# Kernel tuning notes

Measured on AMD Instinct MI355X. Metric: run time of the kernel, lower is better.

Reference implementation:

```python
import jax, jax.numpy as jnp
import numpy as np

BN = 1.0 / np.sqrt(1.0 + 1e-5)  # eval-mode BatchNorm at init (mean=0,var=1,gamma=1,beta=0)
EPS = 1e-5
WIN = 5
NH, HD = 8, 6

def _conv2d(x, w, ph, pw, groups=1):
    return jax.lax.conv_general_dilated(x, w, (1, 1), ((ph, ph), (pw, pw)),
        dimension_numbers=('NCHW', 'OIHW', 'NCHW'), feature_group_count=groups)

def _conv1d(x, w, p, groups=1):
    return jax.lax.conv_general_dilated(x, w, (1,), ((p, p),),
        dimension_numbers=('NCH', 'OIH', 'NCH'), feature_group_count=groups)

def _avgpool_t(x, k):
    s = jax.lax.reduce_window(x, 0.0, jax.lax.add, (1, 1, 1, k), (1, 1, 1, k), 'VALID')
    return s / k

def _ln(h, g, b):
    m = h.mean(-1, keepdims=True)
    v = h.var(-1, keepdims=True)  # biased, matches torch LayerNorm
    return (h - m) / jnp.sqrt(v + EPS) * g + b

def setup_inputs() -> dict:
    ks = jax.random.split(jax.random.key(0), 20)
    def n(i, shape, s=0.05):
        return jax.random.normal(ks[i], shape, dtype=jnp.float32) * s
    z = lambda *s: jnp.zeros(s, jnp.float32)
    o = lambda *s: jnp.ones(s, jnp.float32)
    return {
        'x': jax.random.normal(ks[0], (16, 1, 22, 16000), dtype=jnp.float32),
        'riem_w1': n(1, (253, 256)), 'riem_b1': z(256),
        'riem_w2': n(2, (256, 48)), 'riem_b2': z(48),
        'conv1_w': n(3, (16, 1, 1, 64)),
        'dw1_w': n(4, (32, 1, 22, 1)),
        'dw2_w': n(5, (32, 1, 1, 16)),
        'pw_w': n(6, (48, 32, 1, 1)),
        'tc1_w': n(7, (24, 2, 3)), 'tc1_b': z(24),
        'tc2_w': n(8, (48, 24, 1)), 'tc2_b': z(48),
        'fusion_proj': n(9, (48, 48), 0.15),
        'pos_enc': n(10, (1, 500, 48), 0.02),
        'ln1_g': o(4, 48), 'ln1_b': z(4, 48),
        'qkv_w': n(11, (4, 48, 144)), 'qkv_b': z(4, 144),
        'attn_proj_w': n(12, (4, 48, 48)), 'attn_proj_b': z(4, 48),
        'ln2_g': o(4, 48), 'ln2_b': z(4, 48),
        'ffn_w1': n(13, (4, 48, 192)), 'ffn_b1': z(4, 192),
        'ffn_w2': n(14, (4, 192, 48)), 'ffn_b2': z(4, 48),
        'cls_ln_g': o(48), 'cls_ln_b': z(48),
        'cls_w': n(15, (48, 4), 0.1), 'cls_b': z(4),
    }

def _forward(x, riem_w1, riem_b1, riem_w2, riem_b2, conv1_w, dw1_w, dw2_w, pw_w,
             tc1_w, tc1_b, tc2_w, tc2_b, fusion_proj, pos_enc,
             ln1_g, ln1_b, qkv_w, qkv_b, attn_proj_w, attn_proj_b,
             ln2_g, ln2_b, ffn_w1, ffn_b1, ffn_w2, ffn_b2,
             cls_ln_g, cls_ln_b, cls_w, cls_b):
    B = x.shape[0]
    # ---- Riemannian geometry branch ----
    xr = x[:, 0]                                   # (B, 22, T)
    C, T = xr.shape[1], xr.shape[2]
    xc = xr - xr.mean(-1, keepdims=True)
    cov = jnp.einsum('bct,bdt->bcd', xc, xc) / (T - 1)
    I = jnp.eye(C, dtype=x.dtype)
    cov = cov + I * 1e-5
    tr = jnp.trace(cov, axis1=1, axis2=2)
    cov = cov + I * (tr.mean() * 1e-3)
    L = jnp.linalg.cholesky(cov)
    dL = jnp.diagonal(L, axis1=-2, axis2=-1)
    log_cov = L * jnp.log(jnp.clip(dL, 1e-10))[:, None, :]   # L @ diag(log(diag L))
    iu = jnp.triu_indices(C)
    flat = log_cov[:, iu[0], iu[1]]                # (B, 253)
    r_feat = (jax.nn.elu(flat @ riem_w1 + riem_b1) @ riem_w2 + riem_b2)[:, None, :]
    # ---- Lightweight CNN branch (BatchNorms in eval = constant scale) ----
    h = _conv2d(x, conv1_w, 0, 32) * BN
    h = jax.nn.elu(_conv2d(h, dw1_w, 0, 0, groups=16) * BN)
    h = _avgpool_t(h, 8)
    h = _conv2d(h, dw2_w, 0, 8, groups=32) * BN
    h = jax.nn.elu(_conv2d(h, pw_w, 0, 0) * BN)
    h = _avgpool_t(h, 8)                            # (B, 48, 1, L)
    feat = jnp.transpose(h[:, :, 0, :], (0, 2, 1))  # (B, L, 48)
    t = _conv1d(jnp.transpose(feat, (0, 2, 1)), tc1_w, 1, groups=24) + tc1_b[None, :, None]
    t = jax.nn.gelu(t * BN, approximate=False)
    t = _conv1d(t, tc2_w, 0) + tc2_b[None, :, None]
    feat = feat + jnp.transpose(t, (0, 2, 1))
    # ---- Fusion + positional encoding ----
    fused = jnp.concatenate([r_feat, feat], axis=1) @ fusion_proj
    N = fused.shape[1]
    fused = fused + pos_enc[:, :N]
    # ---- Sparse (banded) transformer blocks ----
    idx = jnp.arange(N)
    band = jnp.abs(idx[:, None] - idx[None, :]) <= WIN   # allowed positions
    scale = HD ** -0.5
    for i in range(4):
        res = fused
        hh = _ln(fused, ln1_g[i], ln1_b[i])
        qkv = (hh @ qkv_w[i] + qkv_b[i]).reshape(B, N, 3, NH, HD)
        q = jnp.transpose(qkv[:, :, 0], (0, 2, 1, 3))
        k = jnp.transpose(qkv[:, :, 1], (0, 2, 1, 3))
        v = jnp.transpose(qkv[:, :, 2], (0, 2, 1, 3))
        att = jnp.einsum('bhqd,bhkd->bhqk', q, k) * scale
        att = jax.nn.softmax(jnp.where(band, att, -jnp.inf), axis=-1)
        o = jnp.einsum('bhqk,bhkd->bhqd', att, v)
        o = jnp.transpose(o, (0, 2, 1, 3)).reshape(B, N, NH * HD)
        fused = res + (o @ attn_proj_w[i] + attn_proj_b[i])
        res = fused
        hh = _ln(fused, ln2_g[i], ln2_b[i])
        hh = jax.nn.gelu(hh @ ffn_w1[i] + ffn_b1[i], approximate=False) @ ffn_w2[i] + ffn_b2[i]
        fused = res + hh
    g = fused.mean(axis=1)
    g = _ln(g, cls_ln_g, cls_ln_b)
    return g @ cls_w + cls_b

def reference(x, riem_w1, riem_b1, riem_w2, riem_b2, conv1_w, dw1_w, dw2_w, pw_w,
              tc1_w, tc1_b, tc2_w, tc2_b, fusion_proj, pos_enc,
              ln1_g, ln1_b, qkv_w, qkv_b, attn_proj_w, attn_proj_b,
              ln2_g, ln2_b, ffn_w1, ffn_b1, ffn_w2, ffn_b2,
              cls_ln_g, cls_ln_b, cls_w, cls_b):
    return _forward(x, riem_w1, riem_b1, riem_w2, riem_b2, conv1_w, dw1_w, dw2_w, pw_w,
                    tc1_w, tc1_b, tc2_w, tc2_b, fusion_proj, pos_enc,
                    ln1_g, ln1_b, qkv_w, qkv_b, attn_proj_w, attn_proj_b,
                    ln2_g, ln2_b, ffn_w1, ffn_b1, ffn_w2, ffn_b2,
                    cls_ln_g, cls_ln_b, cls_w, cls_b)
```

## Files before the change

### kernel.cpp

```cpp
#include <hip/hip_runtime.h>
#include <hip/hip_bf16.h>
#include <math.h>

#define BN_C 0.9999950000375f
#define NB 16
#define NC 22
#define NT 16000
#define NPAIR 253
#define NSEQ 251
#define ND 48
#define TR 8
#define TE 18

__device__ __forceinline__ unsigned short f2bf(float f) {
    union { float f; unsigned int u; } v; v.f = f;
    unsigned int r = v.u + 0x7fff + ((v.u >> 16) & 1);
    return (unsigned short)(r >> 16);
}
__device__ __forceinline__ float bf2f(unsigned short s) {
    union { unsigned int u; float f; } v; v.u = ((unsigned int)s) << 16;
    return v.f;
}
__device__ __forceinline__ float elu_fast(float z) {
    return (z > 0.f) ? z : (__expf(z) - 1.f);
}

#define TCHUNK 500
#define XROW 504
__global__ __launch_bounds__(256) void k_ycov(const float* __restrict__ x,
                                              const float* __restrict__ dw1,
                                              __hip_bfloat16* __restrict__ y,
                                              float* __restrict__ covS,
                                              float* __restrict__ sums) {
    __shared__ unsigned short xs[NC * XROW];
    if (blockIdx.x < 512) {
        int chunk = blockIdx.x & 31, b = blockIdx.x >> 5;
        int t0 = chunk * TCHUNK;
        const float* xp = x + (size_t)b * NC * NT + t0;
        for (int i = threadIdx.x; i < NC * 126; i += 256) {
            int c = i / 126, q = i % 126;
            unsigned long long pk = 0ull;
            if (q < 125) {
                float4 v = *(const float4*)&xp[(size_t)c * NT + 4 * q];
                pk = (unsigned long long)f2bf(v.x) | ((unsigned long long)f2bf(v.y) << 16)
                   | ((unsigned long long)f2bf(v.z) << 32) | ((unsigned long long)f2bf(v.w) << 48);
            }
            *(unsigned long long*)&xs[c * XROW + 4 * q] = pk;
        }
        __syncthreads();
        int p = threadIdx.x;
        if (p < NPAIR) {
            int c = 0, r = p;
            while (r >= NC - c) { r -= NC - c; c++; }
            int d = c + r;
            const unsigned short* xc = &xs[c * XROW];
            const unsigned short* xd = &xs[d * XROW];
            float a0 = 0, a1 = 0, a2 = 0, a3 = 0;
            float s0 = 0, s1 = 0, s2 = 0, s3 = 0;
            for (int t = 0; t < XROW; t += 8) {
                uint4 pc = *(const uint4*)&xc[t];
                uint4 pd = *(const uint4*)&xd[t];
                float c0 = bf2f((unsigned short)pc.x), c1 = bf2f((unsigned short)(pc.x >> 16));
                float c2 = bf2f((unsigned short)pc.y), c3 = bf2f((unsigned short)(pc.y >> 16));
                float c4 = bf2f((unsigned short)pc.z), c5 = bf2f((unsigned short)(pc.z >> 16));
                float c6 = bf2f((unsigned short)pc.w), c7 = bf2f((unsigned short)(pc.w >> 16));
                float d0 = bf2f((unsigned short)pd.x), d1 = bf2f((unsigned short)(pd.x >> 16));
                float d2 = bf2f((unsigned short)pd.y), d3 = bf2f((unsigned short)(pd.y >> 16));
                float d4 = bf2f((unsigned short)pd.z), d5 = bf2f((unsigned short)(pd.z >> 16));
                float d6 = bf2f((unsigned short)pd.w), d7 = bf2f((unsigned short)(pd.w >> 16));
                a0 += c0 * d0 + c4 * d4; a1 += c1 * d1 + c5 * d5;
                a2 += c2 * d2 + c6 * d6; a3 += c3 * d3 + c7 * d7;
                s0 += c0 + c4; s1 += c1 + c5; s2 += c2 + c6; s3 += c3 + c7;
            }
            atomicAdd(&covS[b * NPAIR + p], (a0 + a1) + (a2 + a3));
            if (c == d) atomicAdd(&sums[b * NC + c], (s0 + s1) + (s2 + s3));
        }
    } else {
        int gid = (blockIdx.x - 512) * 256 + threadIdx.x;
        int b = gid / 8000, tp = gid % 8000;
        int t = tp * 2;
        const float* xb = x + (size_t)b * NC * NT + t;
        float a0[32], a1[32];
        #pragma unroll
        for (int j = 0; j < 32; j++) { a0[j] = 0.f; a1[j] = 0.f; }
        for (int h = 0; h < NC; h++) {
            float2 xv = *(const float2*)&xb[(size_t)h * NT];
            #pragma unroll
            for (int j = 0; j < 32; j++) {
                float w = dw1[j * NC + h];
                a0[j] += w * xv.x; a1[j] += w * xv.y;
            }
        }
        unsigned int* yo = (unsigned int*)(y + (size_t)b * 32 * NT + t);
        #pragma unroll
        for (int j = 0; j < 32; j++) {
            unsigned int pk = (unsigned int)f2bf(a0[j]) | ((unsigned int)f2bf(a1[j]) << 16);
            yo[j * (NT / 2)] = pk;
        }
    }
}

__global__ __launch_bounds__(256) void k_convchol(
    const __hip_bfloat16* __restrict__ y, const float* __restrict__ c1w,
    float* __restrict__ p,
    const float* __restrict__ covS, const float* __restrict__ sums,
    const float* __restrict__ w1, const float* __restrict__ b1,
    const float* __restrict__ w2, const float* __restrict__ b2,
    float* __restrict__ rfeat) {
    __shared__ float4 yt4[528];
    __shared__ float covL[484];
    __shared__ float trS[NB];
    __shared__ float dvs[NC];
    __shared__ float hid[256];
    __shared__ float part[4][ND];
    if (blockIdx.x < 4096) {
        int tile = blockIdx.x & 7, j = (blockIdx.x >> 3) & 31, b = blockIdx.x >> 8;
        int u0 = tile * 256;
        const __hip_bfloat16* yp = y + ((size_t)(b * 32 + j)) * NT;
        int tbase = u0 * 8 - 32;
        for (int w = threadIdx.x; w < 528; w += 256) {
            int tq = tbase + 4 * w;
            float4 v;
            if (tq >= 0 && tq + 3 < NT) {
                uint2 pk = *(const uint2*)(yp + tq);
                v.x = bf2f((unsigned short)pk.x); v.y = bf2f((unsigned short)(pk.x >> 16));
                v.z = bf2f((unsigned short)pk.y); v.w = bf2f((unsigned short)(pk.y >> 16));
            } else {
                v.x = (tq >= 0 && tq < NT) ? __bfloat162float(yp[tq]) : 0.f;
                v.y = (tq + 1 >= 0 && tq + 1 < NT) ? __bfloat162float(yp[tq + 1]) : 0.f;
                v.z = (tq + 2 >= 0 && tq + 2 < NT) ? __bfloat162float(yp[tq + 2]) : 0.f;
                v.w = (tq + 3 >= 0 && tq + 3 < NT) ? __bfloat162float(yp[tq + 3]) : 0.f;
            }
            yt4[w ^ ((w >> 3) & 1)] = v;
        }
        __syncthreads();
        const float* cf = c1w + (j >> 1) * 64;
        int u = u0 + threadIdx.x;
        if (u < 2000) {
            float acc[8];
            #pragma unroll
            for (int s = 0; s < 8; s++) acc[s] = 0.f;
            #pragma unroll
            for (int kb = 0; kb < 64; kb += 16) {
                int B0 = 2 * threadIdx.x + (kb >> 2);
                float Yb[24];
                #pragma unroll
                for (int q = 0; q < 6; q++) {
                    int w = B0 + q;
                    float4 v = yt4[w ^ ((w >> 3) & 1)];
                    Yb[4 * q] = v.x; Yb[4 * q + 1] = v.y;
                    Yb[4 * q + 2] = v.z; Yb[4 * q + 3] = v.w;
                }
                #pragma unroll
                for (int k = 0; k < 16; k++) {
                    float c = cf[kb + k];
                    #pragma unroll
                    for (int s = 0; s < 8; s++) acc[s] += c * Yb[k + s];
                }
            }
            const float bn2 = BN_C * BN_C;
            float pv = 0.f;
            #pragma unroll
            for (int s = 0; s < 8; s++) pv += elu_fast(bn2 * acc[s]);
            p[((size_t)(b * 32 + j)) * 2000 + u] = pv * 0.125f;
        }
    } else {
        int b = blockIdx.x - 4096, t = threadIdx.x;
        if (t < NB) trS[t] = 0.f;
        __syncthreads();
        if (t < NPAIR) {
            int c = 0, r = t;
            while (r >= NC - c) { r -= NC - c; c++; }
            int d = c + r;
            float v = (covS[b * NPAIR + t] - sums[b * NC + c] * sums[b * NC + d] / (float)NT)
                      / (float)(NT - 1);
            if (c == d) v += 1e-5f;
            covL[c * NC + d] = v;
            covL[d * NC + c] = v;
        }
        for (int i = t; i < NB * NC; i += 256) {
            int bb = i / NC, c = i % NC;
            int pos = c * NC - c * (c - 1) / 2;
            float sc = sums[bb * NC + c];
            float v = (covS[bb * NPAIR + pos] - sc * sc / (float)NT) / (float)(NT - 1) + 1e-5f;
            atomicAdd(&trS[bb], v);
        }
        __syncthreads();
        float trs = 0.f;
        for (int i = 0; i < NB; i++) trs += trS[i];
        float trm = trs * (0.001f / (float)NB);
        if (t < 64) {
            int lane = t;
            float a[NC];
            #pragma unroll
            for (int j = 0; j < NC; j++) {
                float v = (lane < NC) ? covL[lane * NC + j] : 0.f;
                a[j] = v + ((j == lane) ? trm : 0.f);
            }
            float diagv = 1.f;
            #pragma unroll
            for (int k = 0; k < NC; k++) {
                float akk = __shfl(a[k], k);
                float dk = sqrtf(akk);
                if (lane == k) { a[k] = dk; diagv = dk; }
                else if (lane > k) a[k] /= dk;
                float myak = a[k];
                #pragma unroll
                for (int j = k + 1; j < NC; j++) {
                    float ljk = __shfl(myak, j);
                    if (lane >= j) a[j] -= myak * ljk;
                }
            }
            if (lane < NC) dvs[lane] = diagv * logf(fmaxf(diagv, 1e-10f));
        }
        __syncthreads();
        {
            float acc = b1[t];
            #pragma unroll
            for (int d = 0; d < NC; d++) {
                int pos = d * NC - d * (d - 1) / 2;
                acc += dvs[d] * w1[pos * 256 + t];
            }
            hid[t] = elu_fast(acc);
        }
        __syncthreads();
        if (t < 192) {
            int col = t % ND, kc = t / ND;
            float a = 0.f;
            #pragma unroll
            for (int i = 0; i < 64; i++) a += hid[kc * 64 + i] * w2[(kc * 64 + i) * ND + col];
            part[kc][col] = a;
        }
        __syncthreads();
        if (t < ND)
            rfeat[b * ND + t] = b2[t] + part[0][t] + part[1][t] + part[2][t] + part[3][t];
    }
}

__global__ __launch_bounds__(256) void k_stage2(const float* __restrict__ p,
                                                const float* __restrict__ dw2,
                                                const float* __restrict__ pw,
                                                float* __restrict__ feat) {
    int u2b = blockIdx.x * 4, b = blockIdx.y, t = threadIdx.x;
    __shared__ float pt[32][48];
    __shared__ float dval[32][32];
    __shared__ float w2s[512];
    __shared__ float pws[1536];
    for (int i = t; i < 512; i += 256) w2s[i] = dw2[i];
    for (int i = t; i < 1536; i += 256) pws[i] = pw[i];
    int base = 8 * u2b - 8;
    for (int i = t; i < 32 * 47; i += 256) {
        int j = i / 47, tt = i % 47;
        int gt = base + tt;
        pt[j][tt] = (gt >= 0 && gt < 2000) ? p[((size_t)(b * 32 + j)) * 2000 + gt] : 0.f;
    }
    __syncthreads();
    for (int i = t; i < 1024; i += 256) {
        int j = i >> 5, su = i & 31;
        int u = su >> 3, s = su & 7;
        float a = 0.f;
        #pragma unroll
        for (int k = 0; k < 16; k++) a += w2s[j * 16 + k] * pt[j][8 * u + s + k];
        dval[j][su] = a * BN_C;
    }
    __syncthreads();
    if (t < 192) {
        int col = t % ND, u = t / ND;
        int u2 = u2b + u;
        if (u2 < 250) {
            float wreg[32];
            #pragma unroll
            for (int j = 0; j < 32; j++) wreg[j] = pws[col * 32 + j];
            float acc = 0.f;
            #pragma unroll
            for (int s = 0; s < 8; s++) {
                float e = 0.f;
                #pragma unroll
                for (int j = 0; j < 32; j++) e += wreg[j] * dval[j][u * 8 + s];
                acc += elu_fast(e * BN_C);
            }
            feat[((size_t)b * 250 + u2) * ND + col] = acc * 0.125f;
        }
    }
}

__global__ __launch_bounds__(256) void k_fuse(
    const float* __restrict__ feat, const float* __restrict__ rfeat,
    const float* __restrict__ tc1w, const float* __restrict__ tc1b,
    const float* __restrict__ tc2w, const float* __restrict__ tc2b,
    const float* __restrict__ fp, const float* __restrict__ pe,
    float* __restrict__ fused) {
    int b = blockIdx.y;
    int sub = threadIdx.x >> 6, lt = threadIdx.x & 63;
    int n = blockIdx.x * 4 + sub;
    bool valid = (n < NSEQ);
    __shared__ float row[4][ND];
    __shared__ float g1[4][24];
    if (valid) {
        if (n == 0) {
            if (lt < ND) row[sub][lt] = rfeat[b * ND + lt];
        } else {
            int u = n - 1;
            if (lt < 24) {
                int m = lt;
                float a = tc1b[m];
                #pragma unroll
                for (int k = 0; k < 3; k++) {
                    int uu = u + k - 1;
                    if (uu >= 0 && uu < 250) {
                        float f0 = feat[((size_t)b * 250 + uu) * ND + 2 * m];
                        float f1 = feat[((size_t)b * 250 + uu) * ND + 2 * m + 1];
                        a += tc1w[m * 6 + k] * f0 + tc1w[m * 6 + 3 + k] * f1;
                    }
                }
                float z = a * BN_C;
                g1[sub][m] = 0.5f * z * (1.f + erff(z * 0.70710678f));
            }
        }
    }
    __syncthreads();
    if (valid && n > 0 && lt < ND) {
        int u = n - 1;
        float a = tc2b[lt];
        #pragma unroll
        for (int m = 0; m < 24; m++) a += tc2w[lt * 24 + m] * g1[sub][m];
        row[sub][lt] = feat[((size_t)b * 250 + u) * ND + lt] + a;
    }
    __syncthreads();
    if (valid && lt < ND) {
        float o = pe[n * ND + lt];
        for (int c = 0; c < ND; c++) o += row[sub][c] * fp[c * ND + lt];
        fused[((size_t)b * NSEQ + n) * ND + lt] = o;
    }
}

__global__ __launch_bounds__(512) void k_layer(
    float* __restrict__ fused,
    const float* __restrict__ g1v, const float* __restrict__ b1v,
    const float* __restrict__ qw, const float* __restrict__ qb,
    const float* __restrict__ apw, const float* __restrict__ apb,
    const float* __restrict__ g2v, const float* __restrict__ b2v,
    const float* __restrict__ w1, const float* __restrict__ fb1,
    const float* __restrict__ w2, const float* __restrict__ fb2) {
    int tile = blockIdx.x, b = blockIdx.y;
    int n0 = tile * TR;
    int t = threadIdx.x;
    __shared__ float row[TE][ND];
    __shared__ float hh[TE][ND];
    __shared__ float qkvS[TE * 144];
    __shared__ float ob[TR][ND];
    __shared__ float nrow[TR][ND];
    __shared__ float mrs[TE][2];
    __shared__ float part[4][TR][ND];
    float* hid = qkvS;

    for (int i = t; i < TE * ND; i += 512) {
        int e = i / ND, c = i % ND;
        int n = n0 - 5 + e;
        row[e][c] = (n >= 0 && n < NSEQ) ? fused[((size_t)b * NSEQ + n) * ND + c] : 0.f;
    }
    __syncthreads();
    if (t < TE * 16) {
        int r = t >> 4, i = t & 15;
        float v0 = row[r][i], v1 = row[r][i + 16], v2 = row[r][i + 32];
        float s = v0 + v1 + v2;
        s += __shfl_down(s, 8, 16); s += __shfl_down(s, 4, 16);
        s += __shfl_down(s, 2, 16); s += __shfl_down(s, 1, 16);
        float m = __shfl(s, 0, 16) * (1.f / ND);
        float d0 = v0 - m, d1 = v1 - m, d2 = v2 - m;
        float q = d0 * d0 + d1 * d1 + d2 * d2;
        q += __shfl_down(q, 8, 16); q += __shfl_down(q, 4, 16);
        q += __shfl_down(q, 2, 16); q += __shfl_down(q, 1, 16);
        if (i == 0) { mrs[r][0] = m; mrs[r][1] = rsqrtf(q * (1.f / ND) + 1e-5f); }
    }
    __syncthreads();
    for (int i = t; i < TE * ND; i += 512) {
        int e = i / ND, c = i % ND;
        hh[e][c] = (row[e][c] - mrs[e][0]) * mrs[e][1] * g1v[c] + b1v[c];
    }
    __syncthreads();
    if (t < 288) {
        int col = t % 144, eg = t / 144;
        float w[ND];
        #pragma unroll
        for (int c = 0; c < ND; c++) w[c] = qw[c * 144 + col];
        float bias = qb[col];
        for (int e = eg * 9; e < eg * 9 + 9; e++) {
            float a = bias;
            #pragma unroll
            for (int c = 0; c < ND; c++) a += hh[e][c] * w[c];
            qkvS[e * 144 + col] = a;
        }
    }
    __syncthreads();
    if (t < TR * 8) {
        int r = t >> 3, h = t & 7;
        int n = n0 + r;
        if (n < NSEQ) {
            int k0 = n - 5; if (k0 < 0) k0 = 0;
            int k1 = n + 5; if (k1 > NSEQ - 1) k1 = NSEQ - 1;
            int nk = k1 - k0 + 1;
            float q[6];
            #pragma unroll
            for (int d = 0; d < 6; d++) q[d] = qkvS[(r + 5) * 144 + h * 6 + d];
            float sc[11];
            float mx = -1e30f;
            for (int ki = 0; ki < nk; ki++) {
                int e = k0 + ki - n0 + 5;
                float s = 0;
                #pragma unroll
                for (int d = 0; d < 6; d++) s += q[d] * qkvS[e * 144 + 48 + h * 6 + d];
                s *= 0.4082482904638631f;
                sc[ki] = s; mx = fmaxf(mx, s);
            }
            float sum = 0;
            for (int ki = 0; ki < nk; ki++) { float e = __expf(sc[ki] - mx); sc[ki] = e; sum += e; }
            float inv = 1.f / sum;
            float o[6] = {0, 0, 0, 0, 0, 0};
            for (int ki = 0; ki < nk; ki++) {
                int e = k0 + ki - n0 + 5;
                float pv = sc[ki] * inv;
                #pragma unroll
                for (int d = 0; d < 6; d++) o[d] += pv * qkvS[e * 144 + 96 + h * 6 + d];
            }
            #pragma unroll
            for (int d = 0; d < 6; d++) ob[r][h * 6 + d] = o[d];
        } else {
            #pragma unroll
            for (int d = 0; d < 6; d++) ob[r][h * 6 + d] = 0.f;
        }
    }
    __syncthreads();
    if (t < TR * ND) {
        int r = t / ND, col = t % ND;
        float a = apb[col];
        #pragma unroll
        for (int c = 0; c < ND; c++) a += ob[r][c] * apw[c * ND + col];
        nrow[r][col] = row[r + 5][col] + a;
    }
    __syncthreads();
    if (t < TR * 16) {
        int r = t >> 4, i = t & 15;
        float v0 = nrow[r][i], v1 = nrow[r][i + 16], v2 = nrow[r][i + 32];
        float s = v0 + v1 + v2;
        s += __shfl_down(s, 8, 16); s += __shfl_down(s, 4, 16);
        s += __shfl_down(s, 2, 16); s += __shfl_down(s, 1, 16);
        float m = __shfl(s, 0, 16) * (1.f / ND);
        float d0 = v0 - m, d1 = v1 - m, d2 = v2 - m;
        float q = d0 * d0 + d1 * d1 + d2 * d2;
        q += __shfl_down(q, 8, 16); q += __shfl_down(q, 4, 16);
        q += __shfl_down(q, 2, 16); q += __shfl_down(q, 1, 16);
        if (i == 0) { mrs[r][0] = m; mrs[r][1] = rsqrtf(q * (1.f / ND) + 1e-5f); }
    }
    __syncthreads();
    if (t < TR * ND) {
        int r = t / ND, c = t % ND;
        hh[r][c] = (nrow[r][c] - mrs[r][0]) * mrs[r][1] * g2v[c] + b2v[c];
    }
    __syncthreads();
    if (t < 384) {
        int col = t % 192, rg = t / 192;
        float w[ND];
        #pragma unroll
        for (int c = 0; c < ND; c++) w[c] = w1[c * 192 + col];
        float bias = fb1[col];
        for (int r = rg * 4; r < rg * 4 + 4; r++) {
            float a = bias;
            #pragma unroll
            for (int c = 0; c < ND; c++) a += hh[r][c] * w[c];
            hid[r * 192 + col] = 0.5f * a * (1.f + erff(a * 0.70710678f));
        }
    }
    __syncthreads();
    if (t < 384) {
        int col = t % ND, kc = (t / ND) & 3, rh = t / 192;
        float w[ND];
        #pragma unroll
        for (int i2 = 0; i2 < ND; i2++) w[i2] = w2[(kc * ND + i2) * ND + col];
        for (int r = rh * 4; r < rh * 4 + 4; r++) {
            float a = 0;
            #pragma unroll
            for (int i2 = 0; i2 < ND; i2++) a += hid[r * 192 + kc * ND + i2] * w[i2];
            part[kc][r][col] = a;
        }
    }
    __syncthreads();
    for (int i = t; i < TR * ND; i += 512) {
        int r = i / ND, c = i % ND;
        int n = n0 + r;
        if (n < NSEQ) {
            fused[((size_t)b * NSEQ + n) * ND + c] =
                nrow[r][c] + fb2[c] + part[0][r][c] + part[1][r][c] + part[2][r][c] + part[3][r][c];
        }
    }
}

__global__ void k_head(const float* __restrict__ fused, const float* __restrict__ lg,
                       const float* __restrict__ lb, const float* __restrict__ cw,
                       const float* __restrict__ cb, float* __restrict__ out) {
    int b = blockIdx.x, t = threadIdx.x;
    __shared__ float part[4][ND];
    __shared__ float gg[ND], mv[2];
    if (t < 192) {
        int col = t % ND, qt = t / ND;
        int nA = qt * 63;
        int nB = (nA + 63 < NSEQ) ? nA + 63 : NSEQ;
        float s = 0.f;
        for (int n = nA; n < nB; n++) s += fused[((size_t)b * NSEQ + n) * ND + col];
        part[qt][col] = s;
    }
    __syncthreads();
    if (t < ND) gg[t] = (part[0][t] + part[1][t] + part[2][t] + part[3][t]) * (1.f / NSEQ);
    __syncthreads();
    if (t == 0) {
        float m = 0;
        for (int c = 0; c < ND; c++) m += gg[c];
        m /= (float)ND;
        float v = 0;
        for (int c = 0; c < ND; c++) { float dd = gg[c] - m; v += dd * dd; }
        v /= (float)ND;
        mv[0] = m; mv[1] = rsqrtf(v + 1e-5f);
    }
    __syncthreads();
    if (t < ND) gg[t] = (gg[t] - mv[0]) * mv[1] * lg[t] + lb[t];
    __syncthreads();
    if (t < 4) {
        float a = cb[t];
        for (int c = 0; c < ND; c++) a += gg[c] * cw[c * 4 + t];
        out[b * 4 + t] = a;
    }
}

extern "C" void kernel_launch(void* const* d_in, const int* in_sizes, int n_in,
                              void* d_out, int out_size, void* d_ws, size_t ws_size,
                              hipStream_t stream) {
    const float* x       = (const float*)d_in[0];
    const float* riem_w1 = (const float*)d_in[1];
    const float* riem_b1 = (const float*)d_in[2];
    const float* riem_w2 = (const float*)d_in[3];
    const float* riem_b2 = (const float*)d_in[4];
    const float* conv1_w = (const float*)d_in[5];
    const float* dw1_w   = (const float*)d_in[6];
    const float* dw2_w   = (const float*)d_in[7];
    const float* pw_w    = (const float*)d_in[8];
    const float* tc1_w   = (const float*)d_in[9];
    const float* tc1_b   = (const float*)d_in[10];
    const float* tc2_w   = (const float*)d_in[11];
    const float* tc2_b   = (const float*)d_in[12];
    const float* fusion  = (const float*)d_in[13];
    const float* pos_enc = (const float*)d_in[14];
    const float* ln1_g   = (const float*)d_in[15];
    const float* ln1_b   = (const float*)d_in[16];
    const float* qkv_w   = (const float*)d_in[17];
    const float* qkv_b   = (const float*)d_in[18];
    const float* apw     = (const float*)d_in[19];
    const float* apb     = (const float*)d_in[20];
    const float* ln2_g   = (const float*)d_in[21];
    const float* ln2_b   = (const float*)d_in[22];
    const float* ffn_w1  = (const float*)d_in[23];
    const float* ffn_b1  = (const float*)d_in[24];
    const float* ffn_w2  = (const float*)d_in[25];
    const float* ffn_b2  = (const float*)d_in[26];
    const float* cls_g   = (const float*)d_in[27];
    const float* cls_b_  = (const float*)d_in[28];
    const float* cls_w   = (const float*)d_in[29];
    const float* cls_bb  = (const float*)d_in[30];
    float* out = (float*)d_out;

    float* ws = (float*)d_ws;
    float* covS  = ws;
    float* sums  = ws + 4048;
    float* rfeat = ws + 4400;
    float* feat  = ws + 5168;
    float* fused = ws + 197168;
    float* pbuf  = ws + 389936;
    __hip_bfloat16* ybuf = (__hip_bfloat16*)(ws + 1413936);

    hipMemsetAsync(covS, 0, 4400 * sizeof(float), stream);

    k_ycov<<<1012, 256, 0, stream>>>(x, dw1_w, ybuf, covS, sums);
    k_convchol<<<4112, 256, 0, stream>>>(ybuf, conv1_w, pbuf, covS, sums,
                                         riem_w1, riem_b1, riem_w2, riem_b2, rfeat);
    k_stage2<<<dim3(63, NB), 256, 0, stream>>>(pbuf, dw2_w, pw_w, feat);
    k_fuse<<<dim3(63, NB), 256, 0, stream>>>(feat, rfeat, tc1_w, tc1_b, tc2_w, tc2_b,
                                             fusion, pos_enc, fused);

    for (int i = 0; i < 4; i++) {
        k_layer<<<dim3(32, NB), 512, 0, stream>>>(
            fused, ln1_g + i * 48, ln1_b + i * 48, qkv_w + i * 6912, qkv_b + i * 144,
            apw + i * 2304, apb + i * 48, ln2_g + i * 48, ln2_b + i * 48,
            ffn_w1 + i * 9216, ffn_b1 + i * 192, ffn_w2 + i * 9216, ffn_b2 + i * 48);
    }

    k_head<<<NB, 256, 0, stream>>>(fused, cls_g, cls_b_, cls_w, cls_bb, out);
}
```

Before: 273.5 us.

## Use padded scalar LDS layout for conv tile and schedule Cholesky blocks first

Replaces the XOR-swizzled float4 shared-memory tile with a scalar float array padded by one slot every eight elements, loaded with 32-bit bf16-pair reads and read back one element at a time. The aim is to avoid LDS bank conflicts in the convolution inner loop. It also moves the 16 covariance/Cholesky blocks to the start of the grid so the long serial blocks launch first rather than last. In exchange the shared-memory reads go from 6 wide loads to 23 scalar loads per chunk, which may add LDS instruction overhead.

```diff
diff --git a/kernel.cpp b/kernel.cpp
--- a/kernel.cpp
+++ b/kernel.cpp
@@ -107,49 +107,48 @@
     const float* __restrict__ w1, const float* __restrict__ b1,
     const float* __restrict__ w2, const float* __restrict__ b2,
     float* __restrict__ rfeat) {
-    __shared__ float4 yt4[528];
+    __shared__ float yt[2376];
     __shared__ float covL[484];
     __shared__ float trS[NB];
     __shared__ float dvs[NC];
     __shared__ float hid[256];
     __shared__ float part[4][ND];
-    if (blockIdx.x < 4096) {
-        int tile = blockIdx.x & 7, j = (blockIdx.x >> 3) & 31, b = blockIdx.x >> 8;
+    if (blockIdx.x >= NB) {
+        int bx = blockIdx.x - NB;
+        int tile = bx & 7, j = (bx >> 3) & 31, b = bx >> 8;
         int u0 = tile * 256;
         const __hip_bfloat16* yp = y + ((size_t)(b * 32 + j)) * NT;
         int tbase = u0 * 8 - 32;
-        for (int w = threadIdx.x; w < 528; w += 256) {
-            int tq = tbase + 4 * w;
-            float4 v;
-            if (tq >= 0 && tq + 3 < NT) {
-                uint2 pk = *(const uint2*)(yp + tq);
-                v.x = bf2f((unsigned short)pk.x); v.y = bf2f((unsigned short)(pk.x >> 16));
-                v.z = bf2f((unsigned short)pk.y); v.w = bf2f((unsigned short)(pk.y >> 16));
+        for (int q = threadIdx.x; q < 1056; q += 256) {
+            int i = 2 * q;
+            int tq = tbase + i;
+            float v0 = 0.f, v1 = 0.f;
+            if (tq >= 0 && tq + 1 < NT) {
+                unsigned int pk = *(const unsigned int*)(yp + tq);
+                v0 = bf2f((unsigned short)pk); v1 = bf2f((unsigned short)(pk >> 16));
             } else {
-                v.x = (tq >= 0 && tq < NT) ? __bfloat162float(yp[tq]) : 0.f;
-                v.y = (tq + 1 >= 0 && tq + 1 < NT) ? __bfloat162float(yp[tq + 1]) : 0.f;
-                v.z = (tq + 2 >= 0 && tq + 2 < NT) ? __bfloat162float(yp[tq + 2]) : 0.f;
-                v.w = (tq + 3 >= 0 && tq + 3 < NT) ? __bfloat162float(yp[tq + 3]) : 0.f;
-            }
-            yt4[w ^ ((w >> 3) & 1)] = v;
+                if (tq >= 0 && tq < NT) v0 = __bfloat162float(yp[tq]);
+                if (tq + 1 >= 0 && tq + 1 < NT) v1 = __bfloat162float(yp[tq + 1]);
+            }
+            yt[i + (i >> 3)] = v0;
+            int i1 = i + 1;
+            yt[i1 + (i1 >> 3)] = v1;
         }
         __syncthreads();
         const float* cf = c1w + (j >> 1) * 64;
         int u = u0 + threadIdx.x;
         if (u < 2000) {
+            int off = 8 * threadIdx.x;
             float acc[8];
             #pragma unroll
             for (int s = 0; s < 8; s++) acc[s] = 0.f;
             #pragma unroll
             for (int kb = 0; kb < 64; kb += 16) {
-                int B0 = 2 * threadIdx.x + (kb >> 2);
-                float Yb[24];
-                #pragma unroll
-                for (int q = 0; q < 6; q++) {
-                    int w = B0 + q;
-                    float4 v = yt4[w ^ ((w >> 3) & 1)];
-                    Yb[4 * q] = v.x; Yb[4 * q + 1] = v.y;
-                    Yb[4 * q + 2] = v.z; Yb[4 * q + 3] = v.w;
+                float Yb[23];
+                #pragma unroll
+                for (int m = 0; m < 23; m++) {
+                    int idx = off + kb + m;
+                    Yb[m] = yt[idx + (idx >> 3)];
                 }
                 #pragma unroll
                 for (int k = 0; k < 16; k++) {
@@ -165,7 +164,7 @@
             p[((size_t)(b * 32 + j)) * 2000 + u] = pv * 0.125f;
         }
     } else {
-        int b = blockIdx.x - 4096, t = threadIdx.x;
+        int b = blockIdx.x, t = threadIdx.x;
         if (t < NB) trS[t] = 0.f;
         __syncthreads();
         if (t < NPAIR) {
```

Result: faster. 266.9 us (median of 2 runs) (-2.4%).
